# Kernel optimization log

Measured on AMD Instinct MI355X. Metric: run time of the kernel, lower is better.

The kernel has to match this reference:

```python
import jax, jax.numpy as jnp
import numpy as np

V, E, H, B, S, C = 50000, 300, 512, 128, 80, 6
HH = 2 * H  # hidden_dim * num_directions (BiDi=True)


def _gru_dir(x, w_ih, w_hh, b_ih, b_hh, reverse):
    # x: (b, t, e) -> (b, t, h); torch nn.GRU cell math
    Bv, T, _ = x.shape
    Hd = w_hh.shape[1]
    xg = jnp.einsum('bte,ge->btg', x, w_ih) + b_ih  # (b, t, 3h)
    if reverse:
        xg = xg[:, ::-1]
    def step(h, xt):
        gi_r, gi_z, gi_n = jnp.split(xt, 3, axis=-1)
        gh_r, gh_z, gh_n = jnp.split(h @ w_hh.T + b_hh, 3, axis=-1)
        r = jax.nn.sigmoid(gi_r + gh_r)
        z = jax.nn.sigmoid(gi_z + gh_z)
        n = jnp.tanh(gi_n + r * gh_n)
        hn = (1.0 - z) * n + z * h
        return hn, hn
    h0 = jnp.zeros((Bv, Hd), x.dtype)
    _, hs = jax.lax.scan(step, h0, jnp.swapaxes(xg, 0, 1))
    hs = jnp.swapaxes(hs, 0, 1)
    if reverse:
        hs = hs[:, ::-1]
    return hs


def _bigru(x, pf, pb):
    return jnp.concatenate([_gru_dir(x, *pf, reverse=False), _gru_dir(x, *pb, reverse=True)], axis=-1)


def _conv1d(x, w, b, d):
    y = jax.lax.conv_general_dilated(x, w, (1,), 'VALID', rhs_dilation=(d,),
                                     dimension_numbers=('NCH', 'OIH', 'NCH'))
    return y + b[None, :, None]


def _bn(x, g, b, m, v):
    # eval-mode BatchNorm1d with running stats
    return (x - m[None, :, None]) * (g[None, :, None] / jnp.sqrt(v[None, :, None] + 1e-5)) + b[None, :, None]


def setup_inputs():
    key = jax.random.key(0)
    ks = iter(jax.random.split(key, 64))
    def W(*shape):
        return jax.random.normal(next(ks), shape, jnp.float32) * 0.02
    inp = {
        'input_batch': jax.random.randint(next(ks), (B, S), 1, V),
        'choices_batch': jax.random.randint(next(ks), (B, 4, C), 1, V),
        'emb_table': W(V, E),
    }
    for p in ('sg', 'cg'):
        for d in ('f', 'b'):
            inp[p + '_wih_' + d] = W(3 * H, E)
            inp[p + '_whh_' + d] = W(3 * H, H)
            inp[p + '_bih_' + d] = W(3 * H)
            inp[p + '_bhh_' + d] = W(3 * H)
    inp['lin_w'] = W(HH, HH * C)
    inp['lin_b'] = W(HH)
    inp['attn_w'] = W(HH, HH)
    inp['attn_b'] = W(HH)
    inp['c11_w'] = W(HH, S, 3);  inp['c11_b'] = W(HH)
    inp['c13_w'] = W(HH, HH, 3); inp['c13_b'] = W(HH)
    inp['c21_w'] = W(HH, HH, 3); inp['c21_b'] = W(HH)
    inp['c23_w'] = W(HH, HH, 3); inp['c23_b'] = W(HH)
    for i in ('1', '2'):
        inp['bn' + i + '_g'] = jnp.ones((HH,), jnp.float32)
        inp['bn' + i + '_b'] = jnp.zeros((HH,), jnp.float32)
        inp['bn' + i + '_m'] = jnp.zeros((HH,), jnp.float32)
        inp['bn' + i + '_v'] = jnp.ones((HH,), jnp.float32)
    inp['gate_wp'] = W(2 * HH, HH)
    inp['gate_wc'] = W(2 * HH, 2 * HH)
    inp['gate_b'] = W(2 * HH)
    inp['out_wp'] = W(2 * HH, HH)
    inp['out_b'] = W(2 * HH)
    return inp


def reference(input_batch, choices_batch, emb_table,
              sg_wih_f, sg_whh_f, sg_bih_f, sg_bhh_f, sg_wih_b, sg_whh_b, sg_bih_b, sg_bhh_b,
              cg_wih_f, cg_whh_f, cg_bih_f, cg_bhh_f, cg_wih_b, cg_whh_b, cg_bih_b, cg_bhh_b,
              lin_w, lin_b, attn_w, attn_b,
              c11_w, c11_b, c13_w, c13_b, c21_w, c21_b, c23_w, c23_b,
              bn1_g, bn1_b, bn1_m, bn1_v, bn2_g, bn2_b, bn2_m, bn2_v,
              gate_wp, gate_wc, gate_b, out_wp, out_b):
    # --- encode passage: embedding + BiGRU (dropout is eval-mode identity) ---
    sent = _bigru(emb_table[input_batch],
                  (sg_wih_f, sg_whh_f, sg_bih_f, sg_bhh_f),
                  (sg_wih_b, sg_whh_b, sg_bih_b, sg_bhh_b))  # (B, S, 2h)
    cgf = (cg_wih_f, cg_whh_f, cg_bih_f, cg_bhh_f)
    cgb = (cg_wih_b, cg_whh_b, cg_bih_b, cg_bhh_b)

    def choice_vec(tok):  # (B, C) -> (B, 2h)
        g = _bigru(emb_table[tok], cgf, cgb)               # (B, C, 2h)
        return g.reshape(g.shape[0], -1) @ lin_w.T + lin_b

    cvs = [choice_vec(choices_batch[:, i]) for i in range(4)]

    # --- AttnReader: shared Wh/bh, per-choice softmax attention over seq ---
    Wh = jnp.einsum('bsh,hg->bsg', sent, attn_w)  # (B, S, 2h)
    bh = sent @ attn_b                            # (B, S)

    def attn_read(cv):
        a = jax.nn.softmax(jnp.einsum('bsg,bg->bs', Wh, cv) + bh, axis=1)
        return jnp.einsum('bs,bsh->bh', a, sent)  # (B, 2h)

    pars = [attn_read(cv) for cv in cvs]

    # --- IDCNN: Conv1d treats seq dim S as channels (faithful to source) ---
    x = jax.nn.relu(_bn(_conv1d(sent, c11_w, c11_b, 1), bn1_g, bn1_b, bn1_m, bn1_v))
    x = _conv1d(x, c13_w, c13_b, 3)
    x = jax.nn.relu(_bn(_conv1d(x, c21_w, c21_b, 1), bn2_g, bn2_b, bn2_m, bn2_v))
    x = _conv1d(x, c23_w, c23_b, 3)
    P = jnp.max(x, axis=2)  # AdaptiveMaxPool1d(1) + squeeze -> (B, 2h)

    Cs = [jnp.concatenate([cv, par], axis=1) for cv, par in zip(cvs, pars)]  # (B, 4h)

    # --- PointerNet (note: source bug makes out1..out4 all equal C1WP+bC1) ---
    WP = P @ gate_wp.T          # (B, 4h)
    WP_out = P @ out_wp.T       # (B, 4h)
    Cd1 = Cs[0] * jax.nn.sigmoid(WP + Cs[0] @ gate_wc.T + gate_b)
    o1 = jnp.sum(Cd1 * WP_out, axis=1, keepdims=True) + (Cd1 @ out_b)[:, None]  # (B, 1)
    return jnp.concatenate([o1, o1, o1, o1], axis=1)  # (B, 4)
```

## Files before the change

kernel.cpp:

```cpp
#include <hip/hip_runtime.h>

typedef unsigned int u32;
typedef unsigned short u16;
typedef __attribute__((ext_vector_type(4))) float f32x4;
typedef __attribute__((ext_vector_type(8))) short bf16x8;

#define DEV static __device__ __forceinline__

DEV float sigf(float x){ return 1.0f/(1.0f + expf(-x)); }

DEV u16 f2bf(float x){
  u32 u = __float_as_uint(x);
  u32 r = (u + 0x7FFFu + ((u >> 16) & 1u)) >> 16;
  return (u16)r;
}

DEV u32 encf(float f){
  u32 u = __float_as_uint(f);
  return (u & 0x80000000u) ? ~u : (u | 0x80000000u);
}
DEV float decf(u32 e){
  return (e & 0x80000000u) ? __uint_as_float(e ^ 0x80000000u) : __uint_as_float(~e);
}

DEV void gload16(const void* g, void* l){
  __builtin_amdgcn_global_load_lds((const __attribute__((address_space(1))) u32*)g,
                                   (__attribute__((address_space(3))) u32*)l, 16, 0, 0);
}

__global__ __launch_bounds__(256,2) void gemm_bf16(
    const u16* __restrict__ A, const u16* __restrict__ A2,
    const u16* __restrict__ B,
    const float* __restrict__ bias, const float* __restrict__ bias2,
    float* __restrict__ C, float* __restrict__ C2, int ldc,
    int Kp, int ksteps)
{
  __shared__ u16 lds[(128 + 128)*32];
  char* ldsc = (char*)&lds[0];
  const int Boff = 128*64;
  const int tid = threadIdx.x;
  const int l = tid & 63, w = tid >> 6;
  const int n0 = blockIdx.x * 128, m0 = blockIdx.y * 128;
  const u16* Ause = blockIdx.z ? A2 : A;
  const float* buse = blockIdx.z ? bias2 : bias;
  float* Cuse = blockIdx.z ? C2 : C;
  const int wr = w >> 1, wc = w & 1;
  const int lr = l & 15, g = l >> 4;

  f32x4 acc[4][4];
  #pragma unroll
  for (int i=0;i<4;++i)
    #pragma unroll
    for (int j=0;j<4;++j) acc[i][j] = f32x4{0.f,0.f,0.f,0.f};

  for (int ks = 0; ks < ksteps; ++ks) {
    const int i0 = ks*32;
    __syncthreads();
    #pragma unroll
    for (int r = 0; r < 2; ++r) {
      const int rr = w*2 + r;
      const int c = rr*64 + l;
      const int row = c >> 2, bpos = c & 3;
      const int ib = bpos ^ ((row>>1) & 3);
      gload16(Ause + ((size_t)(m0 + row)*Kp + (i0 + ib*8)), ldsc + rr*1024);
      gload16(B    + ((size_t)(n0 + row)*Kp + (i0 + ib*8)), ldsc + Boff + rr*1024);
    }
    __syncthreads();
    bf16x8 af[4], bfr[4];
    #pragma unroll
    for (int m=0;m<4;++m){
      int o = wr*64 + m*16 + lr;
      af[m] = *(const bf16x8*)(ldsc + o*64 + ((g ^ ((o>>1)&3))<<4));
    }
    #pragma unroll
    for (int n=0;n<4;++n){
      int pr = wc*64 + n*16 + lr;
      bfr[n] = *(const bf16x8*)(ldsc + Boff + pr*64 + ((g ^ ((pr>>1)&3))<<4));
    }
    #pragma unroll
    for (int m=0;m<4;++m)
      #pragma unroll
      for (int n=0;n<4;++n)
        acc[m][n] = __builtin_amdgcn_mfma_f32_16x16x32_bf16(af[m], bfr[n], acc[m][n], 0,0,0);
  }

  #pragma unroll
  for (int m=0;m<4;++m){
    int mm = m0 + wr*64 + m*16 + g*4;
    f32x4 bv = *(const f32x4*)(buse + mm);
    #pragma unroll
    for (int n=0;n<4;++n){
      int p = n0 + wc*64 + n*16 + lr;
      f32x4 v;
      #pragma unroll
      for (int r2=0;r2<4;++r2) v[r2] = acc[m][n][r2] + bv[r2];
      *(f32x4*)(Cuse + (size_t)p*ldc + mm) = v;
    }
  }
}

__global__ __launch_bounds__(256,2) void gemm_bf16_sk(
    const u16* __restrict__ A, const u16* __restrict__ B,
    float* __restrict__ C, int ldc, int Kp, int kpc)
{
  __shared__ u16 lds[(128 + 128)*32];
  char* ldsc = (char*)&lds[0];
  const int Boff = 128*64;
  const int tid = threadIdx.x;
  const int l = tid & 63, w = tid >> 6;
  const int n0 = blockIdx.x * 128, m0 = blockIdx.y * 128;
  const int ks0 = blockIdx.z * kpc;
  const int wr = w >> 1, wc = w & 1;
  const int lr = l & 15, g = l >> 4;

  f32x4 acc[4][4];
  #pragma unroll
  for (int i=0;i<4;++i)
    #pragma unroll
    for (int j=0;j<4;++j) acc[i][j] = f32x4{0.f,0.f,0.f,0.f};

  for (int ks = 0; ks < kpc; ++ks) {
    const int i0 = (ks0 + ks)*32;
    __syncthreads();
    #pragma unroll
    for (int r = 0; r < 2; ++r) {
      const int rr = w*2 + r;
      const int c = rr*64 + l;
      const int row = c >> 2, bpos = c & 3;
      const int ib = bpos ^ ((row>>1) & 3);
      gload16(A + ((size_t)(m0 + row)*Kp + (i0 + ib*8)), ldsc + rr*1024);
      gload16(B + ((size_t)(n0 + row)*Kp + (i0 + ib*8)), ldsc + Boff + rr*1024);
    }
    __syncthreads();
    bf16x8 af[4], bfr[4];
    #pragma unroll
    for (int m=0;m<4;++m){
      int o = wr*64 + m*16 + lr;
      af[m] = *(const bf16x8*)(ldsc + o*64 + ((g ^ ((o>>1)&3))<<4));
    }
    #pragma unroll
    for (int n=0;n<4;++n){
      int pr = wc*64 + n*16 + lr;
      bfr[n] = *(const bf16x8*)(ldsc + Boff + pr*64 + ((g ^ ((pr>>1)&3))<<4));
    }
    #pragma unroll
    for (int m=0;m<4;++m)
      #pragma unroll
      for (int n=0;n<4;++n)
        acc[m][n] = __builtin_amdgcn_mfma_f32_16x16x32_bf16(af[m], bfr[n], acc[m][n], 0,0,0);
  }

  #pragma unroll
  for (int m=0;m<4;++m){
    int mm = m0 + wr*64 + m*16 + g*4;
    #pragma unroll
    for (int n=0;n<4;++n){
      int p = n0 + wc*64 + n*16 + lr;
      float* dst = C + (size_t)p*ldc + mm;
      #pragma unroll
      for (int r2=0;r2<4;++r2) atomicAdd(dst + r2, acc[m][n][r2]);
    }
  }
}

__global__ void initc(float* __restrict__ C, const float* __restrict__ bias,
                      int total, int mmask)
{
  int i = blockIdx.x*256 + threadIdx.x;
  if (i < total) C[i] = bias ? bias[i & mmask] : 0.f;
}

__global__ __launch_bounds__(256) void gru_step(
    const float* __restrict__ xg0, const float* __restrict__ xg1,
    const float* __restrict__ whh0, const float* __restrict__ whh1,
    const float* __restrict__ bhh0, const float* __restrict__ bhh1,
    float* __restrict__ hs, int S, int t)
{
  __shared__ float hL[32*520];
  __shared__ float wL[48*132];
  const int tid = threadIdx.x;
  const int tj = tid & 15, tb = tid >> 4;
  const int jg = blockIdx.x;
  const int b0 = blockIdx.y*32;
  const int dir = blockIdx.z;
  const int l = tid & 63, w = tid >> 6;
  const float* xg  = dir ? xg1  : xg0;
  const float* whh = dir ? whh1 : whh0;
  const float* bhh = dir ? bhh1 : bhh0;
  const int tt = dir ? (S-1-t) : t;
  const int j = jg*16 + tj;

  float accr[2], accz[2], accn[2];
  {
    float br = bhh[j], bz = bhh[512+j], bn = bhh[1024+j];
    accr[0]=br; accr[1]=br; accz[0]=bz; accz[1]=bz; accn[0]=bn; accn[1]=bn;
  }

  if (t > 0){
    const int tp = dir ? (tt+1) : (tt-1);
    #pragma unroll
    for (int rr = 0; rr < 8; ++rr){
      int row = w*8 + rr;
      const float* srcb = hs + ((size_t)(b0+row)*S + tp)*1024 + dir*512;
      gload16(srcb + l*4,       (char*)hL + (size_t)(row*520)*4);
      gload16(srcb + 256 + l*4, (char*)hL + (size_t)(row*520 + 256)*4);
    }
    for (int c = 0; c < 4; ++c){
      const int k0 = c*128;
      __syncthreads();
      #pragma unroll
      for (int i = 0; i < 6; ++i){
        int qidx = tid + i*256;
        int row = qidx >> 5, q = qidx & 31;
        int grow = (row>>4)*512 + jg*16 + (row & 15);
        f32x4 v = *(const f32x4*)(whh + (size_t)grow*512 + k0 + q*4);
        *(f32x4*)(wL + row*132 + q*4) = v;
      }
      __syncthreads();
      #pragma unroll 4
      for (int q = 0; q < 32; ++q){
        f32x4 ha  = *(const f32x4*)(hL + (2*tb  )*520 + k0 + q*4);
        f32x4 hb  = *(const f32x4*)(hL + (2*tb+1)*520 + k0 + q*4);
        f32x4 wr4 = *(const f32x4*)(wL + tj*132      + q*4);
        f32x4 wz4 = *(const f32x4*)(wL + (16+tj)*132 + q*4);
        f32x4 wn4 = *(const f32x4*)(wL + (32+tj)*132 + q*4);
        #pragma unroll
        for (int e = 0; e < 4; ++e){
          accr[0] += ha[e]*wr4[e]; accz[0] += ha[e]*wz4[e]; accn[0] += ha[e]*wn4[e];
          accr[1] += hb[e]*wr4[e]; accz[1] += hb[e]*wz4[e]; accn[1] += hb[e]*wn4[e];
        }
      }
    }
  }

  #pragma unroll
  for (int bi = 0; bi < 2; ++bi){
    int lb = 2*tb + bi;
    int b = b0 + lb;
    size_t xbase = ((size_t)b*S + tt)*1536;
    float gir = xg[xbase + j], giz = xg[xbase + 512 + j], gin = xg[xbase + 1024 + j];
    float hp = (t>0) ? hL[lb*520 + j] : 0.f;
    float r = sigf(gir + accr[bi]);
    float z = sigf(giz + accz[bi]);
    float n = tanhf(gin + r*accn[bi]);
    hs[((size_t)b*S + tt)*1024 + dir*512 + j] = (1.f - z)*n + z*hp;
  }
}

__global__ void transpose_sent(const float* __restrict__ sent, u16* __restrict__ sentT)
{
  __shared__ float tl[80][65];
  int b = blockIdx.y, h0 = blockIdx.x*64;
  for (int idx = threadIdx.x; idx < 80*64; idx += 256){
    int s = idx >> 6, hh = idx & 63;
    tl[s][hh] = sent[((size_t)b*80 + s)*1024 + h0 + hh];
  }
  __syncthreads();
  for (int idx = threadIdx.x; idx < 64*96; idx += 256){
    int hh = idx / 96, s = idx % 96;
    sentT[((size_t)b*1024 + h0 + hh)*96 + s] = (s < 80) ? f2bf(tl[s][hh]) : (u16)0;
  }
}

__global__ void attn_scores(const float* __restrict__ sent, const float* __restrict__ u,
                            const float* __restrict__ attn_b, float* __restrict__ sc)
{
  int wid = blockIdx.x*4 + (threadIdx.x >> 6);
  int lane = threadIdx.x & 63;
  const float* row = sent + (size_t)wid*1024;
  const float* ub = u + (size_t)(wid/80)*1024;
  float acc = 0.f;
  for (int h = lane; h < 1024; h += 64) acc += row[h]*(ub[h] + attn_b[h]);
  #pragma unroll
  for (int m = 32; m; m >>= 1) acc += __shfl_xor(acc, m);
  if (lane == 0) sc[wid] = acc;
}

__global__ void softmax80(const float* __restrict__ sc, float* __restrict__ a)
{
  int b = blockIdx.x, l = threadIdx.x;
  float v0 = sc[b*80 + l];
  float v1 = (l < 16) ? sc[b*80 + 64 + l] : -1e30f;
  float mx = fmaxf(v0, v1);
  #pragma unroll
  for (int m = 32; m; m >>= 1) mx = fmaxf(mx, __shfl_xor(mx, m));
  float e0 = expf(v0 - mx);
  float e1 = (l < 16) ? expf(v1 - mx) : 0.f;
  float s = e0 + e1;
  #pragma unroll
  for (int m = 32; m; m >>= 1) s += __shfl_xor(s, m);
  float inv = 1.f/s;
  a[b*80 + l] = e0*inv;
  if (l < 16) a[b*80 + 64 + l] = e1*inv;
}

__global__ void par_cs0(const float* __restrict__ a, const float* __restrict__ sent,
                        const float* __restrict__ cv, float* __restrict__ Cs0)
{
  int b = blockIdx.x;
  for (int h = threadIdx.x; h < 1024; h += 256){
    float acc = 0.f;
    for (int s = 0; s < 80; ++s) acc += a[b*80+s]*sent[((size_t)b*80+s)*1024 + h];
    Cs0[(size_t)b*2048 + 1024 + h] = acc;
    Cs0[(size_t)b*2048 + h] = cv[(size_t)b*1024 + h];
  }
}

__global__ void pack_w8(const float* __restrict__ src, u16* __restrict__ dst,
                        int O, int CIs, int CIp)
{
  int i = blockIdx.x*256 + threadIdx.x;
  int cip8 = CIp >> 3;
  if (i >= 3*O*cip8) return;
  int tap = i/(O*cip8); int rem = i%(O*cip8);
  int o = rem/cip8, cb = (rem%cip8)*8;
  u16 ov[8];
  #pragma unroll
  for (int jj=0;jj<8;++jj){
    int ci = cb + jj;
    ov[jj] = (ci < CIs) ? f2bf(src[((size_t)o*CIs + ci)*3 + tap]) : (u16)0;
  }
  uint4 v;
  v.x = (u32)ov[0] | ((u32)ov[1]<<16);
  v.y = (u32)ov[2] | ((u32)ov[3]<<16);
  v.z = (u32)ov[4] | ((u32)ov[5]<<16);
  v.w = (u32)ov[6] | ((u32)ov[7]<<16);
  *(uint4*)(dst + ((size_t)tap*O + o)*CIp + cb) = v;
}

__global__ void pack_wk8(const float* __restrict__ src, u16* __restrict__ dst,
                         int M, int Ks, int Kp)
{
  int i = blockIdx.x*256 + threadIdx.x;
  int kp8 = Kp >> 3;
  if (i >= M*kp8) return;
  int row = i/kp8, kb = (i%kp8)*8;
  const float* s = src + (size_t)row*Ks + kb;
  u16 ov[8];
  #pragma unroll
  for (int jj=0;jj<8;++jj) ov[jj] = (kb+jj < Ks) ? f2bf(s[jj]) : (u16)0;
  uint4 v;
  v.x = (u32)ov[0] | ((u32)ov[1]<<16);
  v.y = (u32)ov[2] | ((u32)ov[3]<<16);
  v.z = (u32)ov[4] | ((u32)ov[5]<<16);
  v.w = (u32)ov[6] | ((u32)ov[7]<<16);
  *(uint4*)(dst + (size_t)row*Kp + kb) = v;
}

__global__ void pack_f2b8(const float* __restrict__ src, u16* __restrict__ dst, int n)
{
  int i = blockIdx.x*256 + threadIdx.x;
  if (i >= (n>>3)) return;
  const float* s = src + (size_t)i*8;
  uint4 v;
  v.x = (u32)f2bf(s[0]) | ((u32)f2bf(s[1])<<16);
  v.y = (u32)f2bf(s[2]) | ((u32)f2bf(s[3])<<16);
  v.z = (u32)f2bf(s[4]) | ((u32)f2bf(s[5])<<16);
  v.w = (u32)f2bf(s[6]) | ((u32)f2bf(s[7])<<16);
  *(uint4*)(dst + (size_t)i*8) = v;
}

__global__ void pack_x8(const float* __restrict__ emb, const int* __restrict__ toks,
                        int rdiv, int rmul, u16* __restrict__ dst, int R)
{
  int i = blockIdx.x*256 + threadIdx.x;
  if (i >= R*40) return;
  int row = i/40, kb = (i%40)*8;
  int tok = toks[(row/rdiv)*rmul + (row%rdiv)];
  const float* s = emb + (size_t)tok*300 + kb;
  u16 ov[8];
  #pragma unroll
  for (int jj=0;jj<8;++jj) ov[jj] = (kb+jj < 300) ? f2bf(s[jj]) : (u16)0;
  uint4 v;
  v.x = (u32)ov[0] | ((u32)ov[1]<<16);
  v.y = (u32)ov[2] | ((u32)ov[3]<<16);
  v.z = (u32)ov[4] | ((u32)ov[5]<<16);
  v.w = (u32)ov[6] | ((u32)ov[7]<<16);
  *(uint4*)(dst + (size_t)row*320 + kb) = v;
}

__global__ void prep_ab(const float* c11b, const float* c13b, const float* c21b, const float* c23b,
                        const float* g1, const float* b1, const float* m1, const float* v1,
                        const float* g2, const float* b2, const float* m2, const float* v2,
                        float* ab)
{
  int i = blockIdx.x*256 + threadIdx.x;
  if (i >= 4096) return;
  int layer = i >> 10, o = i & 1023;
  float al, be;
  if (layer == 0){ al = g1[o]/sqrtf(v1[o]+1e-5f); be = c11b[o]*al + b1[o] - m1[o]*al; }
  else if (layer == 1){ al = 1.f; be = c13b[o]; }
  else if (layer == 2){ al = g2[o]/sqrtf(v2[o]+1e-5f); be = c21b[o]*al + b2[o] - m2[o]*al; }
  else { al = 1.f; be = c23b[o]; }
  ab[layer*2048 + o] = al;
  ab[layer*2048 + 1024 + o] = be;
}

__global__ void init_penc(u32* p){
  int i = blockIdx.x*256 + threadIdx.x;
  if (i < 128*1024) p[i] = encf(-3.3e38f);
}
__global__ void dec_p(const u32* __restrict__ pe, float* __restrict__ pf){
  int i = blockIdx.x*256 + threadIdx.x;
  if (i < 128*1024) pf[i] = decf(pe[i]);
}

#define CONV_PHASE(TAP, BRD, STAGECODE, WAITCODE)                             \
  {                                                                           \
    const char* Ab = ldsc + (((ks3 + (TAP)) & 3) << 14) + aRd;                \
    const char* Bb = ldsc + 65536 + bpar + (BRD);                             \
    bf16x8 af[8], bfr[4];                                                     \
    _Pragma("unroll")                                                         \
    for (int m=0;m<8;++m) af[m] = *(const bf16x8*)(Ab + m*1024);              \
    _Pragma("unroll")                                                         \
    for (int n=0;n<4;++n) bfr[n] = *(const bf16x8*)(Bb + n*1024);             \
    STAGECODE                                                                 \
    WAITCODE                                                                  \
    __builtin_amdgcn_s_setprio(1);                                            \
    _Pragma("unroll")                                                         \
    for (int n=0;n<4;++n)                                                     \
      _Pragma("unroll")                                                       \
      for (int m=0;m<8;++m)                                                   \
        acc[m][n] = __builtin_amdgcn_mfma_f32_16x16x32_bf16(af[m], bfr[n],    \
                                                            acc[m][n],0,0,0); \
    __builtin_amdgcn_s_setprio(0);                                            \
    asm volatile("" ::: "memory");                                            \
    __builtin_amdgcn_s_barrier();                                             \
    asm volatile("" ::: "memory");                                            \
  }

#define STAGE_A(TAP)                                                          \
      {                                                                       \
        char* Adst = ldsc + (((ks3 + (TAP) + 3) & 3) << 14);                  \
        gload16(aptr0 + (size_t)(TAP)*1024*CI, Adst + aLd0);                  \
        gload16(aptr1 + (size_t)(TAP)*1024*CI, Adst + aLd1);                  \
      }

#define STAGE_B                                                               \
      {                                                                       \
        char* Bdst = ldsc + 65536 + (bpar ^ 17408);                           \
        gload16(bptr0, Bdst + bLd0);                                          \
        gload16(bptr1, Bdst + bLd1);                                          \
        if (l < 8) gload16(bptr2, Bdst + bLd2);                               \
      }

__global__ __launch_bounds__(512,2) void conv_mfma(
    const u16* __restrict__ X, long bstrideX,
    const u16* __restrict__ Wt,
    const float* __restrict__ alpha, const float* __restrict__ beta,
    u16* __restrict__ Y, long bstrideY,
    u32* __restrict__ Penc, int b0,
    int P_in, int P_out, int CI, int dil, int ksteps, int mode)
{
  __shared__ u16 lds[50176];
  char* ldsc = (char*)&lds[0];
  const int tid = threadIdx.x;
  const int l = tid & 63, w = tid >> 6;
  const int wg = blockIdx.x + (blockIdx.y<<2) + (blockIdx.z<<4);
  const int id2 = ((wg & 7) << 5) | (wg >> 3);
  const int p0 = (id2 & 3) * 256;
  const int o0 = ((id2 >> 2) & 3) * 256;
  const int bz = id2 >> 4;
  const u16* Xb = X + (size_t)bz * (size_t)bstrideX;
  const int wr = w >> 2, wc = w & 3;
  const int lr = l & 15, g = l >> 4;

  const int aRd  = (wr*128 + lr)*64 + ((g ^ ((lr>>1)&3))<<4);
  const int bRd0 = (wc*64 + lr)*64 + ((g ^ ((lr>>1)&3))<<4);
  const int bRd1 = (wc*64 + lr + dil)*64 + ((g ^ (((lr+dil)>>1)&3))<<4);
  const int bRd2 = (wc*64 + lr + 2*dil)*64 + ((g ^ (((lr+2*dil)>>1)&3))<<4);

  const u16 *aptr0, *aptr1;
  int aLd0, aLd1;
  {
    int c0 = tid,        r0 = c0 >> 2, i0b = (c0 & 3) ^ ((r0>>1)&3);
    int c1 = 512 + tid,  r1 = c1 >> 2, i1b = (c1 & 3) ^ ((r1>>1)&3);
    aptr0 = Wt + ((size_t)(o0 + r0)*CI + i0b*8);  aLd0 = c0*16;
    aptr1 = Wt + ((size_t)(o0 + r1)*CI + i1b*8);  aLd1 = c1*16;
  }
  const u16 *bptr0, *bptr1, *bptr2;
  int bLd0, bLd1, bLd2;
  {
    int c0 = w*136 + l,          r0 = c0 >> 2, i0b = (c0 & 3) ^ ((r0>>1)&3);
    int c1 = w*136 + 64 + l,     r1 = c1 >> 2, i1b = (c1 & 3) ^ ((r1>>1)&3);
    int c2 = w*136 + 128 + (l&7),r2 = c2 >> 2, i2b = (c2 & 3) ^ ((r2>>1)&3);
    int p0c = p0 + r0; p0c = p0c < P_in ? p0c : (P_in-1);
    int p1c = p0 + r1; p1c = p1c < P_in ? p1c : (P_in-1);
    int p2c = p0 + r2; p2c = p2c < P_in ? p2c : (P_in-1);
    bptr0 = Xb + ((size_t)p0c*CI + i0b*8);  bLd0 = c0*16;
    bptr1 = Xb + ((size_t)p1c*CI + i1b*8);  bLd1 = c1*16;
    bptr2 = Xb + ((size_t)p2c*CI + i2b*8);  bLd2 = c2*16;
  }

  f32x4 acc[8][4];
  #pragma unroll
  for (int i=0;i<8;++i)
    #pragma unroll
    for (int j=0;j<4;++j) acc[i][j] = f32x4{0.f,0.f,0.f,0.f};

  {
    gload16(aptr0, ldsc + aLd0);
    gload16(aptr1, ldsc + aLd1);
    gload16(aptr0 + (size_t)1024*CI, ldsc + (1<<14) + aLd0);
    gload16(aptr1 + (size_t)1024*CI, ldsc + (1<<14) + aLd1);
    gload16(aptr0 + (size_t)2048*CI, ldsc + (2<<14) + aLd0);
    gload16(aptr1 + (size_t)2048*CI, ldsc + (2<<14) + aLd1);
    gload16(bptr0, ldsc + 65536 + bLd0);
    gload16(bptr1, ldsc + 65536 + bLd1);
    if (l < 8) gload16(bptr2, ldsc + 65536 + bLd2);
    aptr0 += 32; aptr1 += 32; bptr0 += 32; bptr1 += 32; bptr2 += 32;
  }
  asm volatile("s_waitcnt vmcnt(0)" ::: "memory");
  __builtin_amdgcn_s_barrier();
  asm volatile("" ::: "memory");

  int ks3 = 0;
  for (int ks = 0; ks < ksteps-1; ++ks) {
    const int bpar = (ks & 1) ? 17408 : 0;
    CONV_PHASE(0, bRd0,
      STAGE_A(0) STAGE_B,
      asm volatile("s_waitcnt vmcnt(7)" ::: "memory");)
    CONV_PHASE(1, bRd1,
      STAGE_A(1),
      asm volatile("s_waitcnt vmcnt(7)" ::: "memory");)
    CONV_PHASE(2, bRd2,
      STAGE_A(2)
      { aptr0 += 32; aptr1 += 32; bptr0 += 32; bptr1 += 32; bptr2 += 32; },
      asm volatile("s_waitcnt vmcnt(4)" ::: "memory");)
    ks3 += 3;
  }
  {
    const int bpar = ((ksteps-1) & 1) ? 17408 : 0;
    CONV_PHASE(0, bRd0, {},
      asm volatile("s_waitcnt vmcnt(0)" ::: "memory");)
    CONV_PHASE(1, bRd1, {}, {})
    CONV_PHASE(2, bRd2, {}, {})
  }

  if (mode == 2) {
    #pragma unroll
    for (int m=0;m<8;++m){
      int oo = o0 + wr*128 + m*16 + g*4;
      f32x4 al = *(const f32x4*)(alpha + oo);
      f32x4 be = *(const f32x4*)(beta + oo);
      float vm[4] = {-1e30f,-1e30f,-1e30f,-1e30f};
      #pragma unroll
      for (int n=0;n<4;++n){
        int p = p0 + wc*64 + n*16 + lr;
        bool ok = p < P_out;
        #pragma unroll
        for (int r2=0;r2<4;++r2){
          float v = acc[m][n][r2]*al[r2] + be[r2];
          vm[r2] = ok ? fmaxf(vm[r2], v) : vm[r2];
        }
      }
      #pragma unroll
      for (int r2=0;r2<4;++r2){
        float v = vm[r2];
        #pragma unroll
        for (int mask=1; mask<16; mask<<=1) v = fmaxf(v, __shfl_xor(v, mask));
        if (lr == 0) atomicMax(&Penc[(size_t)(b0+bz)*1024 + oo + r2], encf(v));
      }
    }
  } else {
    #pragma unroll
    for (int m=0;m<8;++m){
      int oo = o0 + wr*128 + m*16 + g*4;
      f32x4 al = *(const f32x4*)(alpha + oo);
      f32x4 be = *(const f32x4*)(beta + oo);
      #pragma unroll
      for (int n=0;n<4;++n){
        int p = p0 + wc*64 + n*16 + lr;
        if (p < P_out){
          float v0 = acc[m][n][0]*al[0] + be[0];
          float v1 = acc[m][n][1]*al[1] + be[1];
          float v2 = acc[m][n][2]*al[2] + be[2];
          float v3 = acc[m][n][3]*al[3] + be[3];
          if (mode == 0){ v0=fmaxf(v0,0.f); v1=fmaxf(v1,0.f); v2=fmaxf(v2,0.f); v3=fmaxf(v3,0.f); }
          uint2 pk;
          pk.x = (u32)f2bf(v0) | ((u32)f2bf(v1) << 16);
          pk.y = (u32)f2bf(v2) | ((u32)f2bf(v3) << 16);
          *(uint2*)(Y + (size_t)bz*(size_t)bstrideY + (size_t)p*1024 + oo) = pk;
        }
      }
    }
  }
}

__global__ void head_final(const float* __restrict__ Cs0, const float* __restrict__ t1,
                           const float* __restrict__ t2, const float* __restrict__ outb,
                           float* __restrict__ dout)
{
  __shared__ float red[256];
  int b = blockIdx.x;
  float part = 0.f;
  for (int gg = threadIdx.x; gg < 2048; gg += 256){
    float cd = Cs0[(size_t)b*2048+gg] * sigf(t1[(size_t)b*2048+gg]);
    part += cd * (t2[(size_t)b*2048+gg] + outb[gg]);
  }
  red[threadIdx.x] = part;
  __syncthreads();
  for (int s = 128; s > 0; s >>= 1){
    if (threadIdx.x < s) red[threadIdx.x] += red[threadIdx.x + s];
    __syncthreads();
  }
  if (threadIdx.x < 4) dout[b*4 + threadIdx.x] = red[0];
}

extern "C" void kernel_launch(void* const* d_in, const int* in_sizes, int n_in,
                              void* d_out, int out_size, void* d_ws, size_t ws_size,
                              hipStream_t stream)
{
  (void)in_sizes; (void)n_in; (void)out_size; (void)ws_size;
  const int*   input_batch = (const int*)d_in[0];
  const int*   choices     = (const int*)d_in[1];
  const float* emb    = (const float*)d_in[2];
  const float* sgwihf = (const float*)d_in[3];
  const float* sgwhhf = (const float*)d_in[4];
  const float* sgbihf = (const float*)d_in[5];
  const float* sgbhhf = (const float*)d_in[6];
  const float* sgwihb = (const float*)d_in[7];
  const float* sgwhhb = (const float*)d_in[8];
  const float* sgbihb = (const float*)d_in[9];
  const float* sgbhhb = (const float*)d_in[10];
  const float* cgwihf = (const float*)d_in[11];
  const float* cgwhhf = (const float*)d_in[12];
  const float* cgbihf = (const float*)d_in[13];
  const float* cgbhhf = (const float*)d_in[14];
  const float* cgwihb = (const float*)d_in[15];
  const float* cgwhhb = (const float*)d_in[16];
  const float* cgbihb = (const float*)d_in[17];
  const float* cgbhhb = (const float*)d_in[18];
  const float* lin_w  = (const float*)d_in[19];
  const float* lin_b  = (const float*)d_in[20];
  const float* attn_w = (const float*)d_in[21];
  const float* attn_b = (const float*)d_in[22];
  const float* c11w = (const float*)d_in[23];
  const float* c11b = (const float*)d_in[24];
  const float* c13w = (const float*)d_in[25];
  const float* c13b = (const float*)d_in[26];
  const float* c21w = (const float*)d_in[27];
  const float* c21b = (const float*)d_in[28];
  const float* c23w = (const float*)d_in[29];
  const float* c23b = (const float*)d_in[30];
  const float* bn1g = (const float*)d_in[31];
  const float* bn1b = (const float*)d_in[32];
  const float* bn1m = (const float*)d_in[33];
  const float* bn1v = (const float*)d_in[34];
  const float* bn2g = (const float*)d_in[35];
  const float* bn2b = (const float*)d_in[36];
  const float* bn2m = (const float*)d_in[37];
  const float* bn2v = (const float*)d_in[38];
  const float* gatewp = (const float*)d_in[39];
  const float* gatewc = (const float*)d_in[40];
  const float* gateb  = (const float*)d_in[41];
  const float* outwp  = (const float*)d_in[42];
  const float* outb   = (const float*)d_in[43];
  float* dout = (float*)d_out;

  char* ws = (char*)d_ws; size_t off = 0;
  auto alc = [&](size_t n)->char*{ char* p = ws + off; off = (off + n + 255) & ~(size_t)255; return p; };
  float* xg_f  = (float*)alc((size_t)128*80*1536*4);
  float* xg_b  = (float*)alc((size_t)128*80*1536*4);
  float* xg_cf = (float*)alc((size_t)128*6*1536*4);
  float* xg_cb = (float*)alc((size_t)128*6*1536*4);
  float* gh    = (float*)alc((size_t)2*128*1536*4); (void)gh;
  float* sent  = (float*)alc((size_t)128*80*1024*4);
  float* g_c   = (float*)alc((size_t)128*6*1024*4);
  u16*   sentT = (u16*)alc((size_t)128*1024*96*2);
  float* cv    = (float*)alc((size_t)128*1024*4);
  float* uu    = (float*)alc((size_t)128*1024*4);
  float* scb   = (float*)alc((size_t)128*80*4);
  float* aw    = (float*)alc((size_t)128*80*4);
  float* Cs0   = (float*)alc((size_t)128*2048*4);
  u16* W1p = (u16*)alc((size_t)3*1024*96*2);
  u16* W2p = (u16*)alc((size_t)3*1024*1024*2);
  u16* W3p = (u16*)alc((size_t)3*1024*1024*2);
  u16* W4p = (u16*)alc((size_t)3*1024*1024*2);
  float* ab  = (float*)alc((size_t)4*2048*4);
  u32*  Penc = (u32*)alc((size_t)128*1024*4);
  float* Pf  = (float*)alc((size_t)128*1024*4);
  float* t1  = (float*)alc((size_t)128*2048*4);
  float* t2  = (float*)alc((size_t)128*2048*4);
  u16* xbf_s = (u16*)alc((size_t)10240*320*2);
  u16* xbf_c = (u16*)alc((size_t)768*320*2);
  u16* Wsf = (u16*)alc((size_t)1536*320*2);
  u16* Wsb = (u16*)alc((size_t)1536*320*2);
  u16* Wcf = (u16*)alc((size_t)1536*320*2);
  u16* Wcb = (u16*)alc((size_t)1536*320*2);

  char* R1 = (char*)xg_f;
  u16* linw_bf  = (u16*)(R1);
  u16* attnw_bf = (u16*)(R1 + 12582912);
  u16* gcbf     = (u16*)(R1 + 14680064);
  u16* cvbf     = (u16*)(R1 + 16252928);
  const int bc = 16;
  u16* Y0 = (u16*)(R1 + 16515072);
  u16* Y1 = Y0 + (size_t)bc*1024*1024;
  char* R2 = (char*)sent;
  u16* gwp_bf = (u16*)(R2);
  u16* gwc_bf = (u16*)(R2 + 4194304);
  u16* owp_bf = (u16*)(R2 + 12582912);
  u16* Pfbf   = (u16*)(R2 + 16777216);
  u16* Cs0bf  = (u16*)(R2 + 17039360);

  dim3 T(256), T5(512);

  pack_w8<<<dim3((3*1024*12+255)/256), T, 0, stream>>>(c11w, W1p, 1024, 80, 96);
  pack_w8<<<dim3((3*1024*128+255)/256), T, 0, stream>>>(c13w, W2p, 1024, 1024, 1024);
  pack_w8<<<dim3((3*1024*128+255)/256), T, 0, stream>>>(c21w, W3p, 1024, 1024, 1024);
  pack_w8<<<dim3((3*1024*128+255)/256), T, 0, stream>>>(c23w, W4p, 1024, 1024, 1024);
  pack_wk8<<<dim3((1536*40+255)/256), T, 0, stream>>>(sgwihf, Wsf, 1536, 300, 320);
  pack_wk8<<<dim3((1536*40+255)/256), T, 0, stream>>>(sgwihb, Wsb, 1536, 300, 320);
  pack_wk8<<<dim3((1536*40+255)/256), T, 0, stream>>>(cgwihf, Wcf, 1536, 300, 320);
  pack_wk8<<<dim3((1536*40+255)/256), T, 0, stream>>>(cgwihb, Wcb, 1536, 300, 320);
  pack_x8<<<dim3((10240*40+255)/256), T, 0, stream>>>(emb, input_batch, 80, 80, xbf_s, 10240);
  pack_x8<<<dim3((768*40+255)/256), T, 0, stream>>>(emb, choices, 6, 24, xbf_c, 768);
  prep_ab<<<16, T, 0, stream>>>(c11b, c13b, c21b, c23b,
                                bn1g,bn1b,bn1m,bn1v, bn2g,bn2b,bn2m,bn2v, ab);
  init_penc<<<512, T, 0, stream>>>(Penc);

  gemm_bf16<<<dim3(80,12,2), T, 0, stream>>>(Wsf, Wsb, xbf_s, sgbihf, sgbihb,
                                             xg_f, xg_b, 1536, 320, 10);
  gemm_bf16<<<dim3(6,12,2), T, 0, stream>>>(Wcf, Wcb, xbf_c, cgbihf, cgbihb,
                                            xg_cf, xg_cb, 1536, 320, 10);

  for (int t = 0; t < 80; ++t)
    gru_step<<<dim3(32,4,2), T, 0, stream>>>(xg_f, xg_b, sgwhhf, sgwhhb,
                                             sgbhhf, sgbhhb, sent, 80, t);
  for (int t = 0; t < 6; ++t)
    gru_step<<<dim3(32,4,2), T, 0, stream>>>(xg_cf, xg_cb, cgwhhf, cgwhhb,
                                             cgbhhf, cgbhhb, g_c, 6, t);

  pack_wk8<<<dim3((1024*768+255)/256), T, 0, stream>>>(lin_w, linw_bf, 1024, 6144, 6144);
  pack_wk8<<<dim3((1024*128+255)/256), T, 0, stream>>>(attn_w, attnw_bf, 1024, 1024, 1024);
  pack_f2b8<<<dim3((128*768+255)/256), T, 0, stream>>>(g_c, gcbf, 128*6144);

  transpose_sent<<<dim3(16,128), T, 0, stream>>>(sent, sentT);

  initc<<<dim3((128*1024+255)/256), T, 0, stream>>>(cv, lin_b, 128*1024, 1023);
  gemm_bf16_sk<<<dim3(1,8,6), T, 0, stream>>>(linw_bf, gcbf, cv, 1024, 6144, 32);
  pack_f2b8<<<dim3((128*128+255)/256), T, 0, stream>>>(cv, cvbf, 128*1024);
  initc<<<dim3((128*1024+255)/256), T, 0, stream>>>(uu, nullptr, 128*1024, 1023);
  gemm_bf16_sk<<<dim3(1,8,2), T, 0, stream>>>(attnw_bf, cvbf, uu, 1024, 1024, 16);
  attn_scores<<<2560, T, 0, stream>>>(sent, uu, attn_b, scb);
  softmax80<<<128, dim3(64), 0, stream>>>(scb, aw);
  par_cs0<<<128, T, 0, stream>>>(aw, sent, cv, Cs0);

  pack_wk8<<<dim3((2048*128+255)/256), T, 0, stream>>>(gatewp, gwp_bf, 2048, 1024, 1024);
  pack_wk8<<<dim3((2048*256+255)/256), T, 0, stream>>>(gatewc, gwc_bf, 2048, 2048, 2048);
  pack_wk8<<<dim3((2048*128+255)/256), T, 0, stream>>>(outwp, owp_bf, 2048, 1024, 1024);
  pack_f2b8<<<dim3((128*256+255)/256), T, 0, stream>>>(Cs0, Cs0bf, 128*2048);

  for (int b0 = 0; b0 < 128; b0 += bc){
    conv_mfma<<<dim3(4,4,bc), T5, 0, stream>>>(sentT + (size_t)b0*1024*96, (long)1024*96,
        W1p, ab+0,    ab+1024, Y0, (long)1024*1024, nullptr, 0, 1024, 1022, 96,   1, 3,  0);
    conv_mfma<<<dim3(4,4,bc), T5, 0, stream>>>(Y0, (long)1024*1024,
        W2p, ab+2048, ab+3072, Y1, (long)1024*1024, nullptr, 0, 1022, 1016, 1024, 3, 32, 1);
    conv_mfma<<<dim3(4,4,bc), T5, 0, stream>>>(Y1, (long)1024*1024,
        W3p, ab+4096, ab+5120, Y0, (long)1024*1024, nullptr, 0, 1016, 1014, 1024, 1, 32, 0);
    conv_mfma<<<dim3(4,4,bc), T5, 0, stream>>>(Y0, (long)1024*1024,
        W4p, ab+6144, ab+7168, nullptr, 0, Penc, b0,          1014, 1008, 1024, 3, 32, 2);
  }
  dec_p<<<512, T, 0, stream>>>(Penc, Pf);
  pack_f2b8<<<dim3((128*128+255)/256), T, 0, stream>>>(Pf, Pfbf, 128*1024);

  initc<<<dim3((128*2048+255)/256), T, 0, stream>>>(t1, gateb, 128*2048, 2047);
  gemm_bf16_sk<<<dim3(1,16,2), T, 0, stream>>>(gwp_bf, Pfbf, t1, 2048, 1024, 16);
  gemm_bf16_sk<<<dim3(1,16,4), T, 0, stream>>>(gwc_bf, Cs0bf, t1, 2048, 2048, 16);
  initc<<<dim3((128*2048+255)/256), T, 0, stream>>>(t2, nullptr, 128*2048, 2047);
  gemm_bf16_sk<<<dim3(1,16,2), T, 0, stream>>>(owp_bf, Pfbf, t2, 2048, 1024, 16);
  head_final<<<128, T, 0, stream>>>(Cs0, t1, t2, outb, dout);
}
```

Before: 3.752 ms.

## Shrink conv MFMA tile to 128x256 with 256-thread blocks

Changes the conv_mfma tile from 256 output channels by 256 positions using 8 waves to 128 channels by 256 positions using 4 waves. LDS drops from about 98KB to about 66KB and the grid doubles along the channel dimension. Each wave now loads more of the B tile, so the load indexing and vmcnt wait counts are reworked. The aim is better occupancy and more blocks in flight, at the cost of reading each input tile twice as often and lower per-block reuse.

Measured after the change: 3.833 ms, median of 2. 1.02x slower.

```diff
diff --git a/kernel.cpp b/kernel.cpp
--- a/kernel.cpp
+++ b/kernel.cpp
@@ -407,8 +407,8 @@
 
 #define CONV_PHASE(TAP, BRD, STAGECODE, WAITCODE)                             \
   {                                                                           \
-    const char* Ab = ldsc + (((ks3 + (TAP)) & 3) << 14) + aRd;                \
-    const char* Bb = ldsc + 65536 + bpar + (BRD);                             \
+    const char* Ab = ldsc + (((ks3 + (TAP)) & 3) << 13) + aRd;                \
+    const char* Bb = ldsc + 32768 + bpar + (BRD);                             \
     bf16x8 af[8], bfr[4];                                                     \
     _Pragma("unroll")                                                         \
     for (int m=0;m<8;++m) af[m] = *(const bf16x8*)(Ab + m*1024);              \
@@ -431,20 +431,22 @@
 
 #define STAGE_A(TAP)                                                          \
       {                                                                       \
-        char* Adst = ldsc + (((ks3 + (TAP) + 3) & 3) << 14);                  \
+        char* Adst = ldsc + (((ks3 + (TAP) + 3) & 3) << 13);                  \
         gload16(aptr0 + (size_t)(TAP)*1024*CI, Adst + aLd0);                  \
         gload16(aptr1 + (size_t)(TAP)*1024*CI, Adst + aLd1);                  \
       }
 
 #define STAGE_B                                                               \
       {                                                                       \
-        char* Bdst = ldsc + 65536 + (bpar ^ 17408);                           \
-        gload16(bptr0, Bdst + bLd0);                                          \
-        gload16(bptr1, Bdst + bLd1);                                          \
-        if (l < 8) gload16(bptr2, Bdst + bLd2);                               \
+        char* Bdst = ldsc + 32768 + (bpar ^ 17408);                           \
+        gload16(bp0, Bdst + bl0);                                             \
+        gload16(bp1, Bdst + bl1);                                             \
+        gload16(bp2, Bdst + bl2);                                             \
+        gload16(bp3, Bdst + bl3);                                             \
+        if (l < 16) gload16(bp4, Bdst + bl4);                                 \
       }
 
-__global__ __launch_bounds__(512,2) void conv_mfma(
+__global__ __launch_bounds__(256,2) void conv_mfma(
     const u16* __restrict__ X, long bstrideX,
     const u16* __restrict__ Wt,
     const float* __restrict__ alpha, const float* __restrict__ beta,
@@ -452,44 +454,46 @@
     u32* __restrict__ Penc, int b0,
     int P_in, int P_out, int CI, int dil, int ksteps, int mode)
 {
-  __shared__ u16 lds[50176];
+  __shared__ u16 lds[33792];
   char* ldsc = (char*)&lds[0];
   const int tid = threadIdx.x;
   const int l = tid & 63, w = tid >> 6;
-  const int wg = blockIdx.x + (blockIdx.y<<2) + (blockIdx.z<<4);
-  const int id2 = ((wg & 7) << 5) | (wg >> 3);
+  const int wg = blockIdx.x + (blockIdx.y<<2) + (blockIdx.z<<5);
+  const int id2 = ((wg & 7) << 6) | (wg >> 3);
   const int p0 = (id2 & 3) * 256;
-  const int o0 = ((id2 >> 2) & 3) * 256;
-  const int bz = id2 >> 4;
+  const int o0 = ((id2 >> 2) & 7) * 128;
+  const int bz = id2 >> 5;
   const u16* Xb = X + (size_t)bz * (size_t)bstrideX;
-  const int wr = w >> 2, wc = w & 3;
   const int lr = l & 15, g = l >> 4;
 
-  const int aRd  = (wr*128 + lr)*64 + ((g ^ ((lr>>1)&3))<<4);
-  const int bRd0 = (wc*64 + lr)*64 + ((g ^ ((lr>>1)&3))<<4);
-  const int bRd1 = (wc*64 + lr + dil)*64 + ((g ^ (((lr+dil)>>1)&3))<<4);
-  const int bRd2 = (wc*64 + lr + 2*dil)*64 + ((g ^ (((lr+2*dil)>>1)&3))<<4);
+  const int aRd  = lr*64 + ((g ^ ((lr>>1)&3))<<4);
+  const int bRd0 = (w*64 + lr)*64 + ((g ^ ((lr>>1)&3))<<4);
+  const int bRd1 = (w*64 + lr + dil)*64 + ((g ^ (((lr+dil)>>1)&3))<<4);
+  const int bRd2 = (w*64 + lr + 2*dil)*64 + ((g ^ (((lr+2*dil)>>1)&3))<<4);
 
   const u16 *aptr0, *aptr1;
   int aLd0, aLd1;
   {
     int c0 = tid,        r0 = c0 >> 2, i0b = (c0 & 3) ^ ((r0>>1)&3);
-    int c1 = 512 + tid,  r1 = c1 >> 2, i1b = (c1 & 3) ^ ((r1>>1)&3);
+    int c1 = 256 + tid,  r1 = c1 >> 2, i1b = (c1 & 3) ^ ((r1>>1)&3);
     aptr0 = Wt + ((size_t)(o0 + r0)*CI + i0b*8);  aLd0 = c0*16;
     aptr1 = Wt + ((size_t)(o0 + r1)*CI + i1b*8);  aLd1 = c1*16;
   }
-  const u16 *bptr0, *bptr1, *bptr2;
-  int bLd0, bLd1, bLd2;
+  const u16 *bp0,*bp1,*bp2,*bp3,*bp4;
+  int bl0,bl1,bl2,bl3,bl4;
   {
-    int c0 = w*136 + l,          r0 = c0 >> 2, i0b = (c0 & 3) ^ ((r0>>1)&3);
-    int c1 = w*136 + 64 + l,     r1 = c1 >> 2, i1b = (c1 & 3) ^ ((r1>>1)&3);
-    int c2 = w*136 + 128 + (l&7),r2 = c2 >> 2, i2b = (c2 & 3) ^ ((r2>>1)&3);
-    int p0c = p0 + r0; p0c = p0c < P_in ? p0c : (P_in-1);
-    int p1c = p0 + r1; p1c = p1c < P_in ? p1c : (P_in-1);
-    int p2c = p0 + r2; p2c = p2c < P_in ? p2c : (P_in-1);
-    bptr0 = Xb + ((size_t)p0c*CI + i0b*8);  bLd0 = c0*16;
-    bptr1 = Xb + ((size_t)p1c*CI + i1b*8);  bLd1 = c1*16;
-    bptr2 = Xb + ((size_t)p2c*CI + i2b*8);  bLd2 = c2*16;
+    const int base = w*272;
+#define BSET(PTR, LD, CC)                                                     \
+    { int c = (CC); int row = c>>2, bpos = c&3;                               \
+      int ib = bpos ^ ((row>>1)&3);                                           \
+      int ps = p0 + row; ps = ps < P_in ? ps : (P_in-1);                      \
+      PTR = Xb + ((size_t)ps*CI + ib*8);  LD = c*16; }
+    BSET(bp0, bl0, base + l)
+    BSET(bp1, bl1, base + 64 + l)
+    BSET(bp2, bl2, base + 128 + l)
+    BSET(bp3, bl3, base + 192 + l)
+    BSET(bp4, bl4, base + 256 + (l & 15))
+#undef BSET
   }
 
   f32x4 acc[8][4];
@@ -501,14 +505,17 @@
   {
     gload16(aptr0, ldsc + aLd0);
     gload16(aptr1, ldsc + aLd1);
-    gload16(aptr0 + (size_t)1024*CI, ldsc + (1<<14) + aLd0);
-    gload16(aptr1 + (size_t)1024*CI, ldsc + (1<<14) + aLd1);
-    gload16(aptr0 + (size_t)2048*CI, ldsc + (2<<14) + aLd0);
-    gload16(aptr1 + (size_t)2048*CI, ldsc + (2<<14) + aLd1);
-    gload16(bptr0, ldsc + 65536 + bLd0);
-    gload16(bptr1, ldsc + 65536 + bLd1);
-    if (l < 8) gload16(bptr2, ldsc + 65536 + bLd2);
-    aptr0 += 32; aptr1 += 32; bptr0 += 32; bptr1 += 32; bptr2 += 32;
+    gload16(aptr0 + (size_t)1024*CI, ldsc + (1<<13) + aLd0);
+    gload16(aptr1 + (size_t)1024*CI, ldsc + (1<<13) + aLd1);
+    gload16(aptr0 + (size_t)2048*CI, ldsc + (2<<13) + aLd0);
+    gload16(aptr1 + (size_t)2048*CI, ldsc + (2<<13) + aLd1);
+    gload16(bp0, ldsc + 32768 + bl0);
+    gload16(bp1, ldsc + 32768 + bl1);
+    gload16(bp2, ldsc + 32768 + bl2);
+    gload16(bp3, ldsc + 32768 + bl3);
+    if (l < 16) gload16(bp4, ldsc + 32768 + bl4);
+    aptr0 += 32; aptr1 += 32;
+    bp0 += 32; bp1 += 32; bp2 += 32; bp3 += 32; bp4 += 32;
   }
   asm volatile("s_waitcnt vmcnt(0)" ::: "memory");
   __builtin_amdgcn_s_barrier();
@@ -519,13 +526,14 @@
     const int bpar = (ks & 1) ? 17408 : 0;
     CONV_PHASE(0, bRd0,
       STAGE_A(0) STAGE_B,
-      asm volatile("s_waitcnt vmcnt(7)" ::: "memory");)
+      asm volatile("s_waitcnt vmcnt(9)" ::: "memory");)
     CONV_PHASE(1, bRd1,
       STAGE_A(1),
-      asm volatile("s_waitcnt vmcnt(7)" ::: "memory");)
+      asm volatile("s_waitcnt vmcnt(9)" ::: "memory");)
     CONV_PHASE(2, bRd2,
       STAGE_A(2)
-      { aptr0 += 32; aptr1 += 32; bptr0 += 32; bptr1 += 32; bptr2 += 32; },
+      { aptr0 += 32; aptr1 += 32;
+        bp0 += 32; bp1 += 32; bp2 += 32; bp3 += 32; bp4 += 32; },
       asm volatile("s_waitcnt vmcnt(4)" ::: "memory");)
     ks3 += 3;
   }
@@ -540,13 +548,13 @@
   if (mode == 2) {
     #pragma unroll
     for (int m=0;m<8;++m){
-      int oo = o0 + wr*128 + m*16 + g*4;
+      int oo = o0 + m*16 + g*4;
       f32x4 al = *(const f32x4*)(alpha + oo);
       f32x4 be = *(const f32x4*)(beta + oo);
       float vm[4] = {-1e30f,-1e30f,-1e30f,-1e30f};
       #pragma unroll
       for (int n=0;n<4;++n){
-        int p = p0 + wc*64 + n*16 + lr;
+        int p = p0 + w*64 + n*16 + lr;
         bool ok = p < P_out;
         #pragma unroll
         for (int r2=0;r2<4;++r2){
@@ -565,12 +573,12 @@
   } else {
     #pragma unroll
     for (int m=0;m<8;++m){
-      int oo = o0 + wr*128 + m*16 + g*4;
+      int oo = o0 + m*16 + g*4;
       f32x4 al = *(const f32x4*)(alpha + oo);
       f32x4 be = *(const f32x4*)(beta + oo);
       #pragma unroll
       for (int n=0;n<4;++n){
-        int p = p0 + wc*64 + n*16 + lr;
+        int p = p0 + w*64 + n*16 + lr;
         if (p < P_out){
           float v0 = acc[m][n][0]*al[0] + be[0];
           float v1 = acc[m][n][1]*al[1] + be[1];
@@ -704,7 +712,7 @@
   u16* Pfbf   = (u16*)(R2 + 16777216);
   u16* Cs0bf  = (u16*)(R2 + 17039360);
 
-  dim3 T(256), T5(512);
+  dim3 T(256);
 
   pack_w8<<<dim3((3*1024*12+255)/256), T, 0, stream>>>(c11w, W1p, 1024, 80, 96);
   pack_w8<<<dim3((3*1024*128+255)/256), T, 0, stream>>>(c13w, W2p, 1024, 1024, 1024);
@@ -753,13 +761,13 @@
   pack_f2b8<<<dim3((128*256+255)/256), T, 0, stream>>>(Cs0, Cs0bf, 128*2048);
 
   for (int b0 = 0; b0 < 128; b0 += bc){
-    conv_mfma<<<dim3(4,4,bc), T5, 0, stream>>>(sentT + (size_t)b0*1024*96, (long)1024*96,
+    conv_mfma<<<dim3(4,8,bc), T, 0, stream>>>(sentT + (size_t)b0*1024*96, (long)1024*96,
         W1p, ab+0,    ab+1024, Y0, (long)1024*1024, nullptr, 0, 1024, 1022, 96,   1, 3,  0);
-    conv_mfma<<<dim3(4,4,bc), T5, 0, stream>>>(Y0, (long)1024*1024,
+    conv_mfma<<<dim3(4,8,bc), T, 0, stream>>>(Y0, (long)1024*1024,
         W2p, ab+2048, ab+3072, Y1, (long)1024*1024, nullptr, 0, 1022, 1016, 1024, 3, 32, 1);
-    conv_mfma<<<dim3(4,4,bc), T5, 0, stream>>>(Y1, (long)1024*1024,
+    conv_mfma<<<dim3(4,8,bc), T, 0, stream>>>(Y1, (long)1024*1024,
         W3p, ab+4096, ab+5120, Y0, (long)1024*1024, nullptr, 0, 1016, 1014, 1024, 1, 32, 0);
-    conv_mfma<<<dim3(4,4,bc), T5, 0, stream>>>(Y0, (long)1024*1024,
+    conv_mfma<<<dim3(4,8,bc), T, 0, stream>>>(Y0, (long)1024*1024,
         W4p, ab+6144, ab+7168, nullptr, 0, Penc, b0,          1014, 1008, 1024, 3, 32, 2);
   }
   dec_p<<<512, T, 0, stream>>>(Penc, Pf);
```
